# Kernel optimization log

Hardware: AMD Instinct MI355X
Metric: run time of the kernel (lower is better)

Reference implementation:

```python
import jax, jax.numpy as jnp
import numpy as np

N, L, IN = 256, 128, 8
H1, H2, OUT = 768, 512, 1


def setup_inputs() -> dict:
    key = jax.random.key(0)
    ks = jax.random.split(key, 13)
    s = 0.02
    p = lambda k, shape: jax.random.normal(k, shape, dtype=jnp.float32) * s
    return {
        "x": jax.random.normal(ks[0], (N, L, IN), dtype=jnp.float32),
        "W_ih1": p(ks[1], (4 * H1, IN + 1)),
        "b_ih1": p(ks[2], (4 * H1,)),
        "W_hh1": p(ks[3], (4 * H1, H1)),
        "b_hh1": p(ks[4], (4 * H1,)),
        "W_ih2": p(ks[5], (4 * H1, H1)),
        "b_ih2": p(ks[6], (4 * H1,)),
        "W_hh2": p(ks[7], (4 * H1, H1)),
        "b_hh2": p(ks[8], (4 * H1,)),
        "W1": p(ks[9], (H2, H1)),
        "b1": p(ks[10], (H2,)),
        "W2": p(ks[11], (OUT, H2)),
        "b2": p(ks[12], (OUT,)),
    }


def _lstm_cell(inp, h, c, W_ih, b_ih, W_hh, b_hh):
    # PyTorch LSTMCell: gates ordered (input, forget, cell, output)
    g = inp @ W_ih.T + b_ih + h @ W_hh.T + b_hh
    i, f, gg, o = jnp.split(g, 4, axis=-1)
    c = jax.nn.sigmoid(f) * c + jax.nn.sigmoid(i) * jnp.tanh(gg)
    h = jax.nn.sigmoid(o) * jnp.tanh(c)
    return h, c


def reference(x, W_ih1, b_ih1, W_hh1, b_hh1, W_ih2, b_ih2, W_hh2, b_hh2, W1, b1, W2, b2):
    Nb = x.shape[0]
    H = W_hh1.shape[1]
    z = jnp.zeros((Nb, H), x.dtype)
    col0 = jnp.zeros((Nb, 1), x.dtype)  # initial_output = initial_implied_storage = 0

    def step(carry, x_t):  # x_t: (N, IN)
        h1, c1, h2, c2, prev_out, prev_store = carry
        cur_store = prev_store + x_t[:, :1] - prev_out  # (N, 1)
        inp = jnp.concatenate([x_t, cur_store], axis=-1)  # (N, IN+1)
        h1, c1 = _lstm_cell(inp, h1, c1, W_ih1, b_ih1, W_hh1, b_hh1)
        h2, c2 = _lstm_cell(h1, h2, c2, W_ih2, b_ih2, W_hh2, b_hh2)
        # dropout_prob = 0 -> dropout layers are identity
        out = jax.nn.relu(h2 @ W1.T + b1) @ W2.T + b2  # (N, 1)
        return (h1, c1, h2, c2, out, cur_store), (out, cur_store)

    _, (outs, stores) = jax.lax.scan(step, (z, z, z, z, col0, col0), jnp.swapaxes(x, 0, 1))
    # (L, N, 1) -> (N, L, 1)
    return jnp.swapaxes(outs, 0, 1), jnp.swapaxes(stores, 0, 1)
```

## Files before the change

### kernel.cpp

```cpp
#include <hip/hip_runtime.h>

typedef unsigned short u16;
typedef unsigned int u32;
typedef __attribute__((ext_vector_type(8))) unsigned short ushort8;
typedef __attribute__((ext_vector_type(4))) float f32x4;
typedef __attribute__((ext_vector_type(2))) float f32x2;
typedef __attribute__((ext_vector_type(4))) unsigned int u32x4;
typedef __attribute__((ext_vector_type(8))) __bf16 bf16x8;

#define N_B 256
#define LSEQ 128
#define AROW 2304
#define NBLK 256

#define MFMA_B16(a, b, c) __builtin_amdgcn_mfma_f32_16x16x32_bf16( \
    __builtin_bit_cast(bf16x8, a), __builtin_bit_cast(bf16x8, b), c, 0, 0, 0)

#define GLLDS(gp, lp) __builtin_amdgcn_global_load_lds( \
    (const __attribute__((address_space(1))) void*)(gp), \
    (__attribute__((address_space(3))) void*)(lp), 16, 0, 0)
#define GLLDS_C(gp, lp) __builtin_amdgcn_global_load_lds( \
    (const __attribute__((address_space(1))) void*)(gp), \
    (__attribute__((address_space(3))) void*)(lp), 16, 0, 17)

#define ATOMIC_LD(p) __hip_atomic_load((p), __ATOMIC_RELAXED, __HIP_MEMORY_SCOPE_AGENT)
#define ATOMIC_ST(p, v) __hip_atomic_store((p), (v), __ATOMIC_RELAXED, __HIP_MEMORY_SCOPE_AGENT)

__device__ __forceinline__ void st16_sc(void* p, u32x4 v) {
  asm volatile("global_store_dwordx4 %0, %1, off sc0 sc1" :: "v"(p), "v"(v) : "memory");
}

#define OFF_BP2   0ull
#define SZ_BP2    (48ull*192*512*2)
#define OFF_BP1   (OFF_BP2 + SZ_BP2)
#define SZ_BP1    (24ull*192*512*2)
#define OFF_W1P   (OFF_BP1 + SZ_BP1)
#define SZ_W1P    (24ull*32*512*2)
#define OFF_WIH1T (OFF_W1P + SZ_W1P)
#define SZ_WIH1T  (9ull*3072*4)
#define OFF_BS1   (OFF_WIH1T + SZ_WIH1T)
#define OFF_BS2   (OFF_BS1 + 3072*4)
#define OFF_W8Q   (OFF_BS2 + 3072*4)
#define OFF_G1P   (OFF_W8Q + 3072*4)
#define SZ_G1P    (256ull*3072*4)
#define OFF_PBUF  (OFF_G1P + SZ_G1P)
#define SZ_PBUF   (256ull*8*4)
#define OFF_ZERO  (OFF_PBUF + SZ_PBUF)
#define OFF_ACAT  OFF_ZERO
#define SZ_ACAT   (256ull*2304*2)
#define OFF_C1    (OFF_ACAT + SZ_ACAT)
#define OFF_C2    (OFF_C1 + 256ull*768*4)
#define OFF_SB    (OFF_C2 + 256ull*768*4)
#define OFF_BAR   (OFF_SB + 1024)
#define SZ_BAR    (128 + 256*32*4)
#define OFF_END   (OFF_BAR + SZ_BAR)
#define ZERO_BYTES (OFF_END - OFF_ZERO)

__device__ __forceinline__ float sigf(float v) { return 1.f / (1.f + __expf(-v)); }
__device__ __forceinline__ float tanhfast(float v) { return 1.f - 2.f / (__expf(2.f * v) + 1.f); }
__device__ __forceinline__ u16 f2bf(float f) {
  union { float f; unsigned u; } v; v.f = f;
  unsigned r = v.u + 0x7fffu + ((v.u >> 16) & 1u);
  return (u16)(r >> 16);
}

struct Params {
  const float* x;
  const u16* Bp2; const u16* Bp1; const u16* W1p;
  const float* Wih1t; const float* bs1; const float* bs2; const float* w8q;
  const float* b1; const float* W2; const float* b2;
  u16* Acat; float* g1q; float* c1; float* c2; float* sb; float* pbuf;
  unsigned* bar;
  float* outs; float* stores;
};

__device__ __forceinline__ void waitflags(const unsigned* f, int n, unsigned target, int tid) {
  if (tid < 64) {
    for (;;) {
      unsigned v = (tid < n) ? ATOMIC_LD(f + tid) : target;
      if (__all((int)(v >= target))) break;
      __builtin_amdgcn_s_sleep(1);
    }
  }
  __syncthreads();
}
__device__ __forceinline__ void setflag(unsigned* f, unsigned v) {
  asm volatile("s_waitcnt vmcnt(0)" ::: "memory");
  __syncthreads();
  if (threadIdx.x == 0) ATOMIC_ST(f, v);
}

__global__ void pack_kernel(const float* __restrict__ Wih1, const float* __restrict__ bih1,
                            const float* __restrict__ Whh1, const float* __restrict__ bhh1,
                            const float* __restrict__ Wih2, const float* __restrict__ bih2,
                            const float* __restrict__ Whh2, const float* __restrict__ bhh2,
                            const float* __restrict__ W1,
                            u16* __restrict__ Bp2, u16* __restrict__ Bp1, u16* __restrict__ W1p,
                            float* __restrict__ Wih1t, float* __restrict__ bs1,
                            float* __restrict__ bs2, float* __restrict__ w8q) {
  const long NB2 = 48l * 192 * 512, NB1 = 24l * 192 * 512, NW1 = 24l * 32 * 512, NT = 9l * 3072;
  const long total = NB2 + NB1 + NW1 + NT + 3072 * 3;
  for (long idx = (long)blockIdx.x * 256 + threadIdx.x; idx < total; idx += (long)gridDim.x * 256) {
    if (idx < NB2) {
      long kt = idx / (192 * 512); long r = idx % (192 * 512);
      int jt = (int)(r / 512); int s = (int)(r % 512);
      int ll = s >> 3, e = s & 7;
      int k = (int)kt * 32 + ((ll >> 4) * 8) + e;
      int j = jt * 16 + (ll & 15);
      float v = (k < 768) ? Wih2[j * 768 + k] : Whh2[j * 768 + k - 768];
      Bp2[idx] = f2bf(v);
    } else if (idx < NB2 + NB1) {
      long i = idx - NB2;
      long kt = i / (192 * 512); long r = i % (192 * 512);
      int jt = (int)(r / 512); int s = (int)(r % 512);
      int ll = s >> 3, e = s & 7;
      int k = (int)kt * 32 + ((ll >> 4) * 8) + e;
      int j = jt * 16 + (ll & 15);
      Bp1[i] = f2bf(Whh1[j * 768 + k]);
    } else if (idx < NB2 + NB1 + NW1) {
      long i = idx - NB2 - NB1;
      long kt = i / (32 * 512); long r = i % (32 * 512);
      int jt = (int)(r / 512); int s = (int)(r % 512);
      int ll = s >> 3, e = s & 7;
      int k = (int)kt * 32 + ((ll >> 4) * 8) + e;
      int j = jt * 16 + (ll & 15);
      W1p[i] = f2bf(W1[j * 768 + k]);
    } else if (idx < NB2 + NB1 + NW1 + NT) {
      long i = idx - NB2 - NB1 - NW1;
      int k = (int)(i / 3072), j = (int)(i % 3072);
      Wih1t[i] = Wih1[j * 9 + k];
    } else {
      long i = idx - NB2 - NB1 - NW1 - NT;
      if (i < 3072) bs1[i] = bih1[i] + bhh1[i];
      else if (i < 6144) { long j = i - 3072; bs2[j] = bih2[j] + bhh2[j]; }
      else {
        long cq = i - 6144; int cc = (int)(cq >> 2), q = (int)(cq & 3);
        w8q[cq] = Wih1[(q * 768 + cc) * 9 + 8];
      }
    }
  }
}

__global__ __launch_bounds__(256) void lstm_fused(Params P) {
  __shared__ ushort8 sbuf[48 * 64];
  __shared__ float xsb[64][8];
  __shared__ float csh[8];
  float (*fbuf)[64][16] = (float(*)[64][16])sbuf;
  const int tid = threadIdx.x, l = tid & 63, w = tid >> 6;
  const int bid = blockIdx.x;
  const int c = bid >> 6, local = bid & 63;
  const int rowbase = c * 64;
  unsigned* cfl = P.bar + 32 + c * 128;

  if (local < 48) {
    const int mg = local;
    setflag(cfl + local, 1u);
    for (int t = 0; t < 128; ++t) {
      const int rdbase = 768 + (t & 1) * 768;
      const int wrbase = 768 + ((t + 1) & 1) * 768;
      auto stage_g2 = [&](int kc, int slot) {
#pragma unroll
        for (int i = 0; i < 4; ++i) {
          int f = w * 4 + i;
          if (f < 8) {
            int kt2 = f >> 2, rt = f & 3, kt = kc * 2 + kt2;
            int col = (kt >= 24) ? (rdbase + (kt - 24) * 32 + ((l >> 4) * 8))
                                 : (kt * 32 + ((l >> 4) * 8));
            const u16* gp = P.Acat + (rowbase + rt * 16 + (l & 15)) * AROW + col;
            GLLDS_C(gp, &sbuf[(slot * 16 + f) * 64]);
          } else {
            int g = f - 8, kt2 = g >> 2, q = g & 3, kt = kc * 2 + kt2;
            const u16* gp = P.Bp2 + (((long)(kt * 192 + q * 48 + mg)) << 9) + l * 8;
            GLLDS(gp, &sbuf[(slot * 16 + f) * 64]);
          }
        }
      };
      auto kc_of = [](int g) { int k = g + 12; return (k >= 24) ? k - 24 : k; };
      waitflags(cfl, 48, (unsigned)(t + 1), tid);
      f32x4 acc[4] = {};
      stage_g2(kc_of(0), 0);
      stage_g2(kc_of(1), 1);
      for (int g = 0; g < 24; ++g) {
        if (g < 22) {
          if (g == 10) waitflags(cfl + 96, 16, (unsigned)(t + 1), tid);
          stage_g2(kc_of(g + 2), (g + 2) % 3);
          asm volatile("s_waitcnt vmcnt(8)" ::: "memory");
        } else if (g == 22) {
          asm volatile("s_waitcnt vmcnt(4)" ::: "memory");
        } else {
          asm volatile("s_waitcnt vmcnt(0)" ::: "memory");
        }
        __builtin_amdgcn_s_barrier();
        __builtin_amdgcn_sched_barrier(0);
        const int base = (g % 3) * 16;
#pragma unroll
        for (int kt2 = 0; kt2 < 2; ++kt2) {
          ushort8 bfr = sbuf[(base + 8 + kt2 * 4 + w) * 64 + l];
#pragma unroll
          for (int rt = 0; rt < 4; ++rt) {
            ushort8 a = sbuf[(base + kt2 * 4 + rt) * 64 + l];
            acc[rt] = MFMA_B16(a, bfr, acc[rt]);
          }
        }
        __builtin_amdgcn_sched_barrier(0);
        __builtin_amdgcn_s_barrier();
      }
#pragma unroll
      for (int rt = 0; rt < 4; ++rt)
#pragma unroll
        for (int reg = 0; reg < 4; ++reg) {
          int rl = rt * 16 + (l >> 4) * 4 + reg;
          fbuf[w][rl][l & 15] = acc[rt][reg] + P.bs2[w * 768 + mg * 16 + (l & 15)];
        }
      __syncthreads();
      for (int p = tid; p < 128; p += 256) {
        int r = p >> 1, half = p & 1;
        int n = rowbase + r, mG = mg * 16 + half * 8;
        f32x4 cold0 = *(const f32x4*)(P.c2 + n * 768 + mG);
        f32x4 cold1 = *(const f32x4*)(P.c2 + n * 768 + mG + 4);
        u32 hp[4];
        f32x4 cnew0, cnew1;
#pragma unroll
        for (int k = 0; k < 8; ++k) {
          int pp = half * 8 + k;
          float gi = fbuf[0][r][pp], gf = fbuf[1][r][pp], gg = fbuf[2][r][pp], go = fbuf[3][r][pp];
          float co = (k < 4) ? cold0[k] : cold1[k - 4];
          float cn = sigf(gf) * co + sigf(gi) * tanhfast(gg);
          float h = sigf(go) * tanhfast(cn);
          if (k < 4) cnew0[k] = cn; else cnew1[k - 4] = cn;
          if (k & 1) hp[k >> 1] |= ((u32)f2bf(h)) << 16; else hp[k >> 1] = f2bf(h);
        }
        *(f32x4*)(P.c2 + n * 768 + mG) = cnew0;
        *(f32x4*)(P.c2 + n * 768 + mG + 4) = cnew1;
        st16_sc(P.Acat + n * AROW + wrbase + mG, *(u32x4*)hp);
      }
      setflag(cfl + local, (unsigned)(t + 2));

      if (local < 32) {
        waitflags(cfl, 48, (unsigned)(t + 2), tid);
        ushort8* fst = sbuf + 1024;
        const int n0f = rowbase + (local >> 3) * 16, cg2 = local & 7, ctg = cg2 * 4 + w;
        const int h2rd = 768 + ((t + 1) & 1) * 768;
#pragma unroll
        for (int i = 0; i < 6; ++i) {
          int cc = w * 6 + i;
          const u16* gp = P.Acat + (n0f + (l & 15)) * AROW + h2rd + cc * 32 + ((l >> 4) * 8);
          GLLDS_C(gp, &fst[cc * 64]);
        }
        asm volatile("s_waitcnt vmcnt(0)" ::: "memory");
        __syncthreads();
        const u16* bbase = P.W1p + ((long)ctg << 9) + l * 8;
        f32x4 facc = {};
#pragma unroll 6
        for (int kt = 0; kt < 24; ++kt) {
          ushort8 a = fst[kt * 64 + l];
          ushort8 bf8 = *reinterpret_cast<const ushort8*>(bbase + kt * 16384);
          facc = MFMA_B16(a, bf8, facc);
        }
        int col = ctg * 16 + (l & 15);
        float w2v = P.W2[col], b1v = P.b1[col];
        float pr[4];
#pragma unroll
        for (int reg = 0; reg < 4; ++reg) pr[reg] = fmaxf(facc[reg] + b1v, 0.f) * w2v;
#pragma unroll
        for (int mm = 1; mm < 16; mm <<= 1)
#pragma unroll
          for (int reg = 0; reg < 4; ++reg) pr[reg] += __shfl_xor(pr[reg], mm);
        if ((l & 15) == 0)
#pragma unroll
          for (int reg = 0; reg < 4; ++reg) fbuf[w][(l >> 4) * 4 + reg][0] = pr[reg];
        __syncthreads();
        if (tid < 16)
          ATOMIC_ST(P.pbuf + (n0f + tid) * 8 + cg2,
                    fbuf[0][tid][0] + fbuf[1][tid][0] + fbuf[2][tid][0] + fbuf[3][tid][0]);
        setflag(cfl + 64 + local, (unsigned)(t + 2));
      }
    }
  } else {
    const int jb = local - 48;
    const int n0 = rowbase + jb * 4;
    const int quad = jb >> 2;
    for (int t = -1; t < 128; ++t) {
      if (t < 127) {
        if (t >= 0) waitflags(cfl + 96, 16, (unsigned)(t + 1), tid);
        for (int p = tid; p < 512; p += 256)
          xsb[p >> 3][p & 7] = P.x[((rowbase + (p >> 3)) * LSEQ + t + 1) * 8 + (p & 7)];
        __syncthreads();
        f32x4 acc[3][4] = {};
        if (t >= 0) {
          auto stage_g1 = [&](int kt, int slot) {
#pragma unroll
            for (int i = 0; i < 4; ++i) {
              int f = w * 4 + i;
              if (f < 4) {
                const u16* gp = P.Acat + (rowbase + f * 16 + (l & 15)) * AROW + kt * 32 + ((l >> 4) * 8);
                GLLDS_C(gp, &sbuf[(slot * 16 + f) * 64]);
              } else {
                int jt_l = f - 4;
                const u16* gp = P.Bp1 + (((long)(kt * 192 + jb * 12 + jt_l)) << 9) + l * 8;
                GLLDS(gp, &sbuf[(slot * 16 + f) * 64]);
              }
            }
          };
          stage_g1(0, 0);
          stage_g1(1, 1);
          for (int kt = 0; kt < 24; ++kt) {
            if (kt < 22) {
              stage_g1(kt + 2, (kt + 2) % 3);
              asm volatile("s_waitcnt vmcnt(8)" ::: "memory");
            } else if (kt == 22) {
              asm volatile("s_waitcnt vmcnt(4)" ::: "memory");
            } else {
              asm volatile("s_waitcnt vmcnt(0)" ::: "memory");
            }
            __builtin_amdgcn_s_barrier();
            __builtin_amdgcn_sched_barrier(0);
            const int base = (kt % 3) * 16;
            ushort8 a_[4];
#pragma unroll
            for (int rt = 0; rt < 4; ++rt) a_[rt] = sbuf[(base + rt) * 64 + l];
#pragma unroll
            for (int jj = 0; jj < 3; ++jj) {
              ushort8 bfr = sbuf[(base + 4 + w * 3 + jj) * 64 + l];
#pragma unroll
              for (int rt = 0; rt < 4; ++rt)
                acc[jj][rt] = MFMA_B16(a_[rt], bfr, acc[jj][rt]);
            }
            __builtin_amdgcn_sched_barrier(0);
            __builtin_amdgcn_s_barrier();
          }
        }
        float wc[3][8], bsv[3];
#pragma unroll
        for (int jj = 0; jj < 3; ++jj) {
          int ct = jb * 12 + w * 3 + jj;
          int col = ct * 16 + (l & 15);
          bsv[jj] = P.bs1[col];
#pragma unroll
          for (int k = 0; k < 8; ++k) wc[jj][k] = P.Wih1t[k * 3072 + col];
        }
#pragma unroll
        for (int rt = 0; rt < 4; ++rt)
#pragma unroll
          for (int reg = 0; reg < 4; ++reg) {
            int rl = rt * 16 + (l >> 4) * 4 + reg;
            int n = rowbase + rl;
            float xv[8];
#pragma unroll
            for (int k = 0; k < 8; ++k) xv[k] = xsb[rl][k];
#pragma unroll
            for (int jj = 0; jj < 3; ++jj) {
              int ct = jb * 12 + w * 3 + jj;
              int cin = (ct - quad * 48) * 16 + (l & 15);
              float v = acc[jj][rt][reg] + bsv[jj];
#pragma unroll
              for (int k = 0; k < 8; ++k) v += xv[k] * wc[jj][k];
              ATOMIC_ST(P.g1q + n * 3072 + cin * 4 + quad, v);
            }
          }
        setflag(cfl + 48 + jb, (unsigned)(t + 2));
      }

      if (t < 127) {
        waitflags(cfl + 48, 16, (unsigned)(t + 2), tid);
#pragma unroll
        for (int i = 0; i < 12; ++i) {
          int f = w * 12 + i;
          const float* gp = P.g1q + n0 * 3072 + f * 256 + l * 4;
          GLLDS_C(gp, (char*)sbuf + f * 1024);
        }
      }
      float ov = 0.f;
      if (t >= 0) {
        waitflags(cfl + 64, 32, (unsigned)(t + 2), tid);
        if (tid < 4) {
          int n = n0 + tid;
          float pb[8];
#pragma unroll
          for (int i = 0; i < 8; ++i) pb[i] = ATOMIC_LD(P.pbuf + n * 8 + i);
          ov = ((pb[0] + pb[1]) + (pb[2] + pb[3])) + ((pb[4] + pb[5]) + (pb[6] + pb[7])) + P.b2[0];
          P.outs[n * LSEQ + t] = ov;
        }
      }
      if (t < 127) {
        if (tid < 4) {
          int n = n0 + tid;
          float cs = P.sb[n] + P.x[(n * LSEQ + t + 1) * 8] - ov;
          P.sb[n] = cs;
          P.stores[n * LSEQ + t + 1] = cs;
          csh[tid] = cs;
        }
        asm volatile("s_waitcnt vmcnt(0)" ::: "memory");
        __syncthreads();
        const int r = tid >> 6, l2 = tid & 63;
        const int n = n0 + r;
        const float* ldsrow = (const float*)sbuf + r * 3072;
        float cs = csh[r];
#pragma unroll
        for (int ci = 0; ci < 6; ++ci) {
          int m = ci * 128 + l2 * 2;
          f32x4 qa = *(const f32x4*)(ldsrow + m * 4);
          f32x4 qb = *(const f32x4*)(ldsrow + m * 4 + 4);
          f32x4 wa = *(const f32x4*)(P.w8q + m * 4);
          f32x4 wb = *(const f32x4*)(P.w8q + m * 4 + 4);
          float ga[4], gb[4];
#pragma unroll
          for (int q = 0; q < 4; ++q) { ga[q] = qa[q] + cs * wa[q]; gb[q] = qb[q] + cs * wb[q]; }
          f32x2 co = *(const f32x2*)(P.c1 + n * 768 + m);
          float cn0 = sigf(ga[1]) * co.x + sigf(ga[0]) * tanhfast(ga[2]);
          float cn1 = sigf(gb[1]) * co.y + sigf(gb[0]) * tanhfast(gb[2]);
          float h0 = sigf(ga[3]) * tanhfast(cn0);
          float h1 = sigf(gb[3]) * tanhfast(cn1);
          f32x2 cn; cn.x = cn0; cn.y = cn1;
          *(f32x2*)(P.c1 + n * 768 + m) = cn;
          u32 pk = (u32)f2bf(h0) | ((u32)f2bf(h1) << 16);
          ATOMIC_ST((u32*)(P.Acat + n * AROW + m), pk);
        }
        setflag(cfl + 96 + jb, (unsigned)(t + 2));
      }
    }
  }
}

extern "C" void kernel_launch(void* const* d_in, const int* in_sizes, int n_in,
                              void* d_out, int out_size, void* d_ws, size_t ws_size,
                              hipStream_t stream) {
  const float* x    = (const float*)d_in[0];
  const float* Wih1 = (const float*)d_in[1];
  const float* bih1 = (const float*)d_in[2];
  const float* Whh1 = (const float*)d_in[3];
  const float* bhh1 = (const float*)d_in[4];
  const float* Wih2 = (const float*)d_in[5];
  const float* bih2 = (const float*)d_in[6];
  const float* Whh2 = (const float*)d_in[7];
  const float* bhh2 = (const float*)d_in[8];
  const float* W1   = (const float*)d_in[9];
  const float* b1   = (const float*)d_in[10];
  const float* W2   = (const float*)d_in[11];
  const float* b2   = (const float*)d_in[12];

  char* ws = (char*)d_ws;
  u16* Bp2 = (u16*)(ws + OFF_BP2);
  u16* Bp1 = (u16*)(ws + OFF_BP1);
  u16* W1p = (u16*)(ws + OFF_W1P);
  float* Wih1t = (float*)(ws + OFF_WIH1T);
  float* bs1 = (float*)(ws + OFF_BS1);
  float* bs2 = (float*)(ws + OFF_BS2);
  float* w8q = (float*)(ws + OFF_W8Q);
  float* g1q = (float*)(ws + OFF_G1P);
  float* pbuf = (float*)(ws + OFF_PBUF);
  u16* Acat = (u16*)(ws + OFF_ACAT);
  float* c1 = (float*)(ws + OFF_C1);
  float* c2 = (float*)(ws + OFF_C2);
  float* sb = (float*)(ws + OFF_SB);
  unsigned* bar = (unsigned*)(ws + OFF_BAR);
  float* outs = (float*)d_out;
  float* stores = outs + N_B * LSEQ;

  pack_kernel<<<2048, 256, 0, stream>>>(Wih1, bih1, Whh1, bhh1, Wih2, bih2, Whh2, bhh2, W1,
                                        Bp2, Bp1, W1p, Wih1t, bs1, bs2, w8q);
  (void)hipMemsetAsync(ws + OFF_ZERO, 0, ZERO_BYTES, stream);

  Params Pr = {x, Bp2, Bp1, W1p, Wih1t, bs1, bs2, w8q, b1, W2, b2,
               Acat, g1q, c1, c2, sb, pbuf, bar, outs, stores};
  lstm_fused<<<NBLK, 256, 0, stream>>>(Pr);
}
```

Before: 3.820 ms.

## Move output MLP into layer-1 blocks and stage gate writes through LDS

```diff
diff --git a/kernel.cpp b/kernel.cpp
--- a/kernel.cpp
+++ b/kernel.cpp
@@ -43,9 +43,7 @@
 #define OFF_W8Q   (OFF_BS2 + 3072*4)
 #define OFF_G1P   (OFF_W8Q + 3072*4)
 #define SZ_G1P    (256ull*3072*4)
-#define OFF_PBUF  (OFF_G1P + SZ_G1P)
-#define SZ_PBUF   (256ull*8*4)
-#define OFF_ZERO  (OFF_PBUF + SZ_PBUF)
+#define OFF_ZERO  (OFF_G1P + SZ_G1P)
 #define OFF_ACAT  OFF_ZERO
 #define SZ_ACAT   (256ull*2304*2)
 #define OFF_C1    (OFF_ACAT + SZ_ACAT)
@@ -69,7 +67,7 @@
   const u16* Bp2; const u16* Bp1; const u16* W1p;
   const float* Wih1t; const float* bs1; const float* bs2; const float* w8q;
   const float* b1; const float* W2; const float* b2;
-  u16* Acat; float* g1q; float* c1; float* c2; float* sb; float* pbuf;
+  u16* Acat; float* g1q; float* c1; float* c2; float* sb;
   unsigned* bar;
   float* outs; float* stores;
 };
@@ -144,6 +142,8 @@
 __global__ __launch_bounds__(256) void lstm_fused(Params P) {
   __shared__ ushort8 sbuf[48 * 64];
   __shared__ float xsb[64][8];
+  __shared__ u16 h2s[4][768];
+  __shared__ float red[4][4];
   __shared__ float csh[8];
   float (*fbuf)[64][16] = (float(*)[64][16])sbuf;
   const int tid = threadIdx.x, l = tid & 63, w = tid >> 6;
@@ -235,51 +235,10 @@
         st16_sc(P.Acat + n * AROW + wrbase + mG, *(u32x4*)hp);
       }
       setflag(cfl + local, (unsigned)(t + 2));
-
-      if (local < 32) {
-        waitflags(cfl, 48, (unsigned)(t + 2), tid);
-        ushort8* fst = sbuf + 1024;
-        const int n0f = rowbase + (local >> 3) * 16, cg2 = local & 7, ctg = cg2 * 4 + w;
-        const int h2rd = 768 + ((t + 1) & 1) * 768;
-#pragma unroll
-        for (int i = 0; i < 6; ++i) {
-          int cc = w * 6 + i;
-          const u16* gp = P.Acat + (n0f + (l & 15)) * AROW + h2rd + cc * 32 + ((l >> 4) * 8);
-          GLLDS_C(gp, &fst[cc * 64]);
-        }
-        asm volatile("s_waitcnt vmcnt(0)" ::: "memory");
-        __syncthreads();
-        const u16* bbase = P.W1p + ((long)ctg << 9) + l * 8;
-        f32x4 facc = {};
-#pragma unroll 6
-        for (int kt = 0; kt < 24; ++kt) {
-          ushort8 a = fst[kt * 64 + l];
-          ushort8 bf8 = *reinterpret_cast<const ushort8*>(bbase + kt * 16384);
-          facc = MFMA_B16(a, bf8, facc);
-        }
-        int col = ctg * 16 + (l & 15);
-        float w2v = P.W2[col], b1v = P.b1[col];
-        float pr[4];
-#pragma unroll
-        for (int reg = 0; reg < 4; ++reg) pr[reg] = fmaxf(facc[reg] + b1v, 0.f) * w2v;
-#pragma unroll
-        for (int mm = 1; mm < 16; mm <<= 1)
-#pragma unroll
-          for (int reg = 0; reg < 4; ++reg) pr[reg] += __shfl_xor(pr[reg], mm);
-        if ((l & 15) == 0)
-#pragma unroll
-          for (int reg = 0; reg < 4; ++reg) fbuf[w][(l >> 4) * 4 + reg][0] = pr[reg];
-        __syncthreads();
-        if (tid < 16)
-          ATOMIC_ST(P.pbuf + (n0f + tid) * 8 + cg2,
-                    fbuf[0][tid][0] + fbuf[1][tid][0] + fbuf[2][tid][0] + fbuf[3][tid][0]);
-        setflag(cfl + 64 + local, (unsigned)(t + 2));
-      }
     }
   } else {
     const int jb = local - 48;
     const int n0 = rowbase + jb * 4;
-    const int quad = jb >> 2;
     for (int t = -1; t < 128; ++t) {
       if (t < 127) {
         if (t >= 0) waitflags(cfl + 96, 16, (unsigned)(t + 1), tid);
@@ -297,7 +256,8 @@
                 GLLDS_C(gp, &sbuf[(slot * 16 + f) * 64]);
               } else {
                 int jt_l = f - 4;
-                const u16* gp = P.Bp1 + (((long)(kt * 192 + jb * 12 + jt_l)) << 9) + l * 8;
+                int q = jt_l / 3, jj = jt_l - q * 3;
+                const u16* gp = P.Bp1 + (((long)(kt * 192 + q * 48 + jb * 3 + jj)) << 9) + l * 8;
                 GLLDS(gp, &sbuf[(slot * 16 + f) * 64]);
               }
             }
@@ -333,35 +293,38 @@
         float wc[3][8], bsv[3];
 #pragma unroll
         for (int jj = 0; jj < 3; ++jj) {
-          int ct = jb * 12 + w * 3 + jj;
-          int col = ct * 16 + (l & 15);
-          bsv[jj] = P.bs1[col];
-#pragma unroll
-          for (int k = 0; k < 8; ++k) wc[jj][k] = P.Wih1t[k * 3072 + col];
-        }
+          int j = w * 768 + (jb * 3 + jj) * 16 + (l & 15);
+          bsv[jj] = P.bs1[j];
+#pragma unroll
+          for (int k = 0; k < 8; ++k) wc[jj][k] = P.Wih1t[k * 3072 + j];
+        }
+        float* eps = (float*)sbuf;
 #pragma unroll
         for (int rt = 0; rt < 4; ++rt)
 #pragma unroll
           for (int reg = 0; reg < 4; ++reg) {
             int rl = rt * 16 + (l >> 4) * 4 + reg;
-            int n = rowbase + rl;
             float xv[8];
 #pragma unroll
             for (int k = 0; k < 8; ++k) xv[k] = xsb[rl][k];
 #pragma unroll
             for (int jj = 0; jj < 3; ++jj) {
-              int ct = jb * 12 + w * 3 + jj;
-              int cin = (ct - quad * 48) * 16 + (l & 15);
               float v = acc[jj][rt][reg] + bsv[jj];
 #pragma unroll
               for (int k = 0; k < 8; ++k) v += xv[k] * wc[jj][k];
-              ATOMIC_ST(P.g1q + n * 3072 + cin * 4 + quad, v);
+              eps[rl * 192 + (jj * 16 + (l & 15)) * 4 + w] = v;
             }
           }
+        __syncthreads();
+#pragma unroll
+        for (int k2 = 0; k2 < 12; ++k2) {
+          int idx = tid + k2 * 256;
+          int row = idx / 48, cl = idx - row * 48;
+          u32x4 v = *(const u32x4*)(eps + row * 192 + cl * 4);
+          st16_sc(P.g1q + (rowbase + row) * 3072 + (jb * 48 + cl) * 4, v);
+        }
         setflag(cfl + 48 + jb, (unsigned)(t + 2));
-      }
-
-      if (t < 127) {
+
         waitflags(cfl + 48, 16, (unsigned)(t + 2), tid);
 #pragma unroll
         for (int i = 0; i < 12; ++i) {
@@ -370,51 +333,90 @@
           GLLDS_C(gp, (char*)sbuf + f * 1024);
         }
       }
-      float ov = 0.f;
+
       if (t >= 0) {
-        waitflags(cfl + 64, 32, (unsigned)(t + 2), tid);
-        if (tid < 4) {
-          int n = n0 + tid;
-          float pb[8];
-#pragma unroll
-          for (int i = 0; i < 8; ++i) pb[i] = ATOMIC_LD(P.pbuf + n * 8 + i);
-          ov = ((pb[0] + pb[1]) + (pb[2] + pb[3])) + ((pb[4] + pb[5]) + (pb[6] + pb[7])) + P.b2[0];
+        waitflags(cfl, 48, (unsigned)(t + 2), tid);
+        const int h2rd = 768 + ((t + 1) & 1) * 768;
+        for (int i = w; i < 6; i += 4) {
+          int bo = i * 1024 + l * 16;
+          int row = bo / 1536, cb = bo - row * 1536;
+          const u16* gp = P.Acat + (n0 + row) * AROW + h2rd + cb / 2;
+          GLLDS_C(gp, (char*)h2s + i * 1024);
+        }
+        asm volatile("s_waitcnt vmcnt(0)" ::: "memory");
+        __syncthreads();
+        f32x4 fa[8] = {};
+        const u16* bb = P.W1p + l * 8;
+        for (int kt = 0; kt < 24; ++kt) {
+          ushort8 a = *(const ushort8*)((const char*)h2s + (l & 3) * 1536 + kt * 64 + ((l >> 4) * 8) * 2);
+#pragma unroll
+          for (int i = 0; i < 8; ++i) {
+            ushort8 b = *(const ushort8*)(bb + (((long)kt * 32 + (w * 8 + i)) << 9));
+            fa[i] = MFMA_B16(a, b, fa[i]);
+          }
+        }
+        float pr[4] = {0.f, 0.f, 0.f, 0.f};
+#pragma unroll
+        for (int i = 0; i < 8; ++i) {
+          int col = (w * 8 + i) * 16 + (l & 15);
+          float b1v = P.b1[col], w2v = P.W2[col];
+#pragma unroll
+          for (int reg = 0; reg < 4; ++reg)
+            pr[reg] += fmaxf(fa[i][reg] + b1v, 0.f) * w2v;
+        }
+#pragma unroll
+        for (int mm = 1; mm < 16; mm <<= 1)
+#pragma unroll
+          for (int reg = 0; reg < 4; ++reg) pr[reg] += __shfl_xor(pr[reg], mm);
+        if (l == 0)
+#pragma unroll
+          for (int reg = 0; reg < 4; ++reg) red[w][reg] = pr[reg];
+        __syncthreads();
+      }
+
+      if (tid < 4) {
+        int n = n0 + tid;
+        float ov = 0.f;
+        if (t >= 0) {
+          ov = red[0][tid] + red[1][tid] + red[2][tid] + red[3][tid] + P.b2[0];
           P.outs[n * LSEQ + t] = ov;
         }
-      }
-      if (t < 127) {
-        if (tid < 4) {
-          int n = n0 + tid;
+        if (t < 127) {
           float cs = P.sb[n] + P.x[(n * LSEQ + t + 1) * 8] - ov;
           P.sb[n] = cs;
           P.stores[n * LSEQ + t + 1] = cs;
           csh[tid] = cs;
         }
+      }
+      if (t < 127) {
         asm volatile("s_waitcnt vmcnt(0)" ::: "memory");
         __syncthreads();
         const int r = tid >> 6, l2 = tid & 63;
         const int n = n0 + r;
         const float* ldsrow = (const float*)sbuf + r * 3072;
         float cs = csh[r];
-#pragma unroll
-        for (int ci = 0; ci < 6; ++ci) {
-          int m = ci * 128 + l2 * 2;
-          f32x4 qa = *(const f32x4*)(ldsrow + m * 4);
-          f32x4 qb = *(const f32x4*)(ldsrow + m * 4 + 4);
-          f32x4 wa = *(const f32x4*)(P.w8q + m * 4);
-          f32x4 wb = *(const f32x4*)(P.w8q + m * 4 + 4);
-          float ga[4], gb[4];
-#pragma unroll
-          for (int q = 0; q < 4; ++q) { ga[q] = qa[q] + cs * wa[q]; gb[q] = qb[q] + cs * wb[q]; }
-          f32x2 co = *(const f32x2*)(P.c1 + n * 768 + m);
-          float cn0 = sigf(ga[1]) * co.x + sigf(ga[0]) * tanhfast(ga[2]);
-          float cn1 = sigf(gb[1]) * co.y + sigf(gb[0]) * tanhfast(gb[2]);
-          float h0 = sigf(ga[3]) * tanhfast(cn0);
-          float h1 = sigf(gb[3]) * tanhfast(cn1);
-          f32x2 cn; cn.x = cn0; cn.y = cn1;
-          *(f32x2*)(P.c1 + n * 768 + m) = cn;
-          u32 pk = (u32)f2bf(h0) | ((u32)f2bf(h1) << 16);
-          ATOMIC_ST((u32*)(P.Acat + n * AROW + m), pk);
+        for (int idx = l2; idx < 96; idx += 64) {
+          int m = idx * 8;
+          u32 hp[4];
+          f32x4 c1v0 = *(const f32x4*)(P.c1 + n * 768 + m);
+          f32x4 c1v1 = *(const f32x4*)(P.c1 + n * 768 + m + 4);
+          f32x4 nc0, nc1;
+#pragma unroll
+          for (int k = 0; k < 8; ++k) {
+            int mm = m + k;
+            f32x4 q = *(const f32x4*)(ldsrow + mm * 4);
+            f32x4 wq = *(const f32x4*)(P.w8q + mm * 4);
+            float g0 = q[0] + cs * wq[0], g1v = q[1] + cs * wq[1];
+            float g2v = q[2] + cs * wq[2], g3v = q[3] + cs * wq[3];
+            float co = (k < 4) ? c1v0[k] : c1v1[k - 4];
+            float cn = sigf(g1v) * co + sigf(g0) * tanhfast(g2v);
+            float h = sigf(g3v) * tanhfast(cn);
+            if (k < 4) nc0[k] = cn; else nc1[k - 4] = cn;
+            if (k & 1) hp[k >> 1] |= ((u32)f2bf(h)) << 16; else hp[k >> 1] = f2bf(h);
+          }
+          *(f32x4*)(P.c1 + n * 768 + m) = nc0;
+          *(f32x4*)(P.c1 + n * 768 + m + 4) = nc1;
+          st16_sc(P.Acat + n * AROW + m, *(u32x4*)hp);
         }
         setflag(cfl + 96 + jb, (unsigned)(t + 2));
       }
@@ -448,7 +450,6 @@
   float* bs2 = (float*)(ws + OFF_BS2);
   float* w8q = (float*)(ws + OFF_W8Q);
   float* g1q = (float*)(ws + OFF_G1P);
-  float* pbuf = (float*)(ws + OFF_PBUF);
   u16* Acat = (u16*)(ws + OFF_ACAT);
   float* c1 = (float*)(ws + OFF_C1);
   float* c2 = (float*)(ws + OFF_C2);
@@ -462,6 +463,6 @@
   (void)hipMemsetAsync(ws + OFF_ZERO, 0, ZERO_BYTES, stream);
 
   Params Pr = {x, Bp2, Bp1, W1p, Wih1t, bs1, bs2, w8q, b1, W2, b2,
-               Acat, g1q, c1, c2, sb, pbuf, bar, outs, stores};
+               Acat, g1q, c1, c2, sb, bar, outs, stores};
   lstm_fused<<<NBLK, 256, 0, stream>>>(Pr);
 }
```

New measurement: 13.36 ms. 250% more time.

## Load B operands into registers with deeper pipelines and vectorize gate1 stores

Applied to the files above, without the earlier changes.

```diff
diff --git a/kernel.cpp b/kernel.cpp
--- a/kernel.cpp
+++ b/kernel.cpp
@@ -29,6 +29,8 @@
 __device__ __forceinline__ void st16_sc(void* p, u32x4 v) {
   asm volatile("global_store_dwordx4 %0, %1, off sc0 sc1" :: "v"(p), "v"(v) : "memory");
 }
+#define LOADB(dst, gp) asm volatile("global_load_dwordx4 %0, %1, off" : "=v"(dst) : "v"(gp))
+#define VMW(N) asm volatile("s_waitcnt vmcnt(" #N ")" ::: "memory")
 
 #define OFF_BP2   0ull
 #define SZ_BP2    (48ull*192*512*2)
@@ -158,53 +160,65 @@
     for (int t = 0; t < 128; ++t) {
       const int rdbase = 768 + (t & 1) * 768;
       const int wrbase = 768 + ((t + 1) & 1) * 768;
-      auto stage_g2 = [&](int kc, int slot) {
-#pragma unroll
-        for (int i = 0; i < 4; ++i) {
-          int f = w * 4 + i;
-          if (f < 8) {
-            int kt2 = f >> 2, rt = f & 3, kt = kc * 2 + kt2;
-            int col = (kt >= 24) ? (rdbase + (kt - 24) * 32 + ((l >> 4) * 8))
-                                 : (kt * 32 + ((l >> 4) * 8));
-            const u16* gp = P.Acat + (rowbase + rt * 16 + (l & 15)) * AROW + col;
-            GLLDS_C(gp, &sbuf[(slot * 16 + f) * 64]);
-          } else {
-            int g = f - 8, kt2 = g >> 2, q = g & 3, kt = kc * 2 + kt2;
-            const u16* gp = P.Bp2 + (((long)(kt * 192 + q * 48 + mg)) << 9) + l * 8;
-            GLLDS(gp, &sbuf[(slot * 16 + f) * 64]);
-          }
+      waitflags(cfl, 48, (unsigned)(t + 1), tid);
+
+      f32x4 acc[4] = {};
+      ushort8 bring[4][2];
+      auto issueA2 = [&](int gi) {
+        const int slot = gi % 6;
+#pragma unroll
+        for (int kt2 = 0; kt2 < 2; ++kt2) {
+          int kt = ((gi < 12) ? gi + 12 : gi - 12) * 2 + kt2;
+          int col = (kt >= 24) ? (rdbase + (kt - 24) * 32 + ((l >> 4) * 8))
+                               : (kt * 32 + ((l >> 4) * 8));
+          const u16* gp = P.Acat + (rowbase + w * 16 + (l & 15)) * AROW + col;
+          GLLDS_C(gp, &sbuf[slot * 512 + (kt2 * 4 + w) * 64]);
         }
       };
-      auto kc_of = [](int g) { int k = g + 12; return (k >= 24) ? k - 24 : k; };
-      waitflags(cfl, 48, (unsigned)(t + 1), tid);
-      f32x4 acc[4] = {};
-      stage_g2(kc_of(0), 0);
-      stage_g2(kc_of(1), 1);
-      for (int g = 0; g < 24; ++g) {
-        if (g < 22) {
-          if (g == 10) waitflags(cfl + 96, 16, (unsigned)(t + 1), tid);
-          stage_g2(kc_of(g + 2), (g + 2) % 3);
-          asm volatile("s_waitcnt vmcnt(8)" ::: "memory");
-        } else if (g == 22) {
-          asm volatile("s_waitcnt vmcnt(4)" ::: "memory");
-        } else {
-          asm volatile("s_waitcnt vmcnt(0)" ::: "memory");
-        }
+      auto baddr2 = [&](int gi, int kt2) -> const u16* {
+        int kt = ((gi < 12) ? gi + 12 : gi - 12) * 2 + kt2;
+        return P.Bp2 + (((long)(kt * 192 + w * 48 + mg)) << 9) + l * 8;
+      };
+      auto g2_step = [&](int g, const ushort8 (&bu)[2]) {
         __builtin_amdgcn_s_barrier();
         __builtin_amdgcn_sched_barrier(0);
-        const int base = (g % 3) * 16;
-#pragma unroll
-        for (int kt2 = 0; kt2 < 2; ++kt2) {
-          ushort8 bfr = sbuf[(base + 8 + kt2 * 4 + w) * 64 + l];
+        const int sb8 = (g % 6) * 512;
+#pragma unroll
+        for (int kt2 = 0; kt2 < 2; ++kt2)
 #pragma unroll
           for (int rt = 0; rt < 4; ++rt) {
-            ushort8 a = sbuf[(base + kt2 * 4 + rt) * 64 + l];
-            acc[rt] = MFMA_B16(a, bfr, acc[rt]);
+            ushort8 a = sbuf[sb8 + (kt2 * 4 + rt) * 64 + l];
+            acc[rt] = MFMA_B16(a, bu[kt2], acc[rt]);
           }
-        }
         __builtin_amdgcn_sched_barrier(0);
-        __builtin_amdgcn_s_barrier();
-      }
+      };
+#pragma unroll
+      for (int p = 0; p < 3; ++p) {
+        issueA2(p);
+        LOADB(bring[p][0], baddr2(p, 0));
+        LOADB(bring[p][1], baddr2(p, 1));
+      }
+      for (int ko = 0; ko < 5; ++ko) {
+#pragma unroll
+        for (int u = 0; u < 4; ++u) {
+          const int g = ko * 4 + u;
+          if (g == 9) waitflags(cfl + 96, 16, (unsigned)(t + 1), tid);
+          issueA2(g + 3);
+          LOADB(bring[(u + 3) & 3][0], baddr2(g + 3, 0));
+          LOADB(bring[(u + 3) & 3][1], baddr2(g + 3, 1));
+          VMW(12);
+          g2_step(g, bring[u]);
+        }
+      }
+      issueA2(23);
+      LOADB(bring[3][0], baddr2(23, 0));
+      LOADB(bring[3][1], baddr2(23, 1));
+      VMW(12); g2_step(20, bring[0]);
+      VMW(8);  g2_step(21, bring[1]);
+      VMW(4);  g2_step(22, bring[2]);
+      VMW(0);  g2_step(23, bring[3]);
+      __syncthreads();
+
 #pragma unroll
       for (int rt = 0; rt < 4; ++rt)
 #pragma unroll
@@ -279,8 +293,8 @@
   } else {
     const int jb = local - 48;
     const int n0 = rowbase + jb * 4;
-    const int quad = jb >> 2;
     for (int t = -1; t < 128; ++t) {
+      float ov = 0.f;
       if (t < 127) {
         if (t >= 0) waitflags(cfl + 96, 16, (unsigned)(t + 1), tid);
         for (int p = tid; p < 512; p += 256)
@@ -288,80 +302,92 @@
         __syncthreads();
         f32x4 acc[3][4] = {};
         if (t >= 0) {
-          auto stage_g1 = [&](int kt, int slot) {
-#pragma unroll
-            for (int i = 0; i < 4; ++i) {
-              int f = w * 4 + i;
-              if (f < 4) {
-                const u16* gp = P.Acat + (rowbase + f * 16 + (l & 15)) * AROW + kt * 32 + ((l >> 4) * 8);
-                GLLDS_C(gp, &sbuf[(slot * 16 + f) * 64]);
-              } else {
-                int jt_l = f - 4;
-                const u16* gp = P.Bp1 + (((long)(kt * 192 + jb * 12 + jt_l)) << 9) + l * 8;
-                GLLDS(gp, &sbuf[(slot * 16 + f) * 64]);
-              }
-            }
+          ushort8 br1[4][3];
+          auto issueA1 = [&](int ki) {
+            const u16* gp = P.Acat + (rowbase + w * 16 + (l & 15)) * AROW + ki * 32 + ((l >> 4) * 8);
+            GLLDS_C(gp, &sbuf[(ki & 7) * 256 + w * 64]);
           };
-          stage_g1(0, 0);
-          stage_g1(1, 1);
-          for (int kt = 0; kt < 24; ++kt) {
-            if (kt < 22) {
-              stage_g1(kt + 2, (kt + 2) % 3);
-              asm volatile("s_waitcnt vmcnt(8)" ::: "memory");
-            } else if (kt == 22) {
-              asm volatile("s_waitcnt vmcnt(4)" ::: "memory");
-            } else {
-              asm volatile("s_waitcnt vmcnt(0)" ::: "memory");
-            }
+          auto baddr1 = [&](int ki, int jj) -> const u16* {
+            return P.Bp1 + (((long)(ki * 192 + w * 48 + jb * 3 + jj)) << 9) + l * 8;
+          };
+          auto g1_step = [&](int kt, const ushort8 (&bu)[3]) {
             __builtin_amdgcn_s_barrier();
             __builtin_amdgcn_sched_barrier(0);
-            const int base = (kt % 3) * 16;
+            const int sb8 = (kt & 7) * 256;
             ushort8 a_[4];
 #pragma unroll
-            for (int rt = 0; rt < 4; ++rt) a_[rt] = sbuf[(base + rt) * 64 + l];
-#pragma unroll
-            for (int jj = 0; jj < 3; ++jj) {
-              ushort8 bfr = sbuf[(base + 4 + w * 3 + jj) * 64 + l];
+            for (int rt = 0; rt < 4; ++rt) a_[rt] = sbuf[sb8 + rt * 64 + l];
+#pragma unroll
+            for (int jj = 0; jj < 3; ++jj)
 #pragma unroll
               for (int rt = 0; rt < 4; ++rt)
-                acc[jj][rt] = MFMA_B16(a_[rt], bfr, acc[jj][rt]);
+                acc[jj][rt] = MFMA_B16(a_[rt], bu[jj], acc[jj][rt]);
+            __builtin_amdgcn_sched_barrier(0);
+          };
+#pragma unroll
+          for (int p = 0; p < 3; ++p) {
+            issueA1(p);
+            LOADB(br1[p][0], baddr1(p, 0));
+            LOADB(br1[p][1], baddr1(p, 1));
+            LOADB(br1[p][2], baddr1(p, 2));
+          }
+          for (int ko = 0; ko < 5; ++ko) {
+#pragma unroll
+            for (int u = 0; u < 4; ++u) {
+              const int kt = ko * 4 + u;
+              issueA1(kt + 3);
+              LOADB(br1[(u + 3) & 3][0], baddr1(kt + 3, 0));
+              LOADB(br1[(u + 3) & 3][1], baddr1(kt + 3, 1));
+              LOADB(br1[(u + 3) & 3][2], baddr1(kt + 3, 2));
+              VMW(12);
+              g1_step(kt, br1[u]);
             }
-            __builtin_amdgcn_sched_barrier(0);
-            __builtin_amdgcn_s_barrier();
           }
+          issueA1(23);
+          LOADB(br1[3][0], baddr1(23, 0));
+          LOADB(br1[3][1], baddr1(23, 1));
+          LOADB(br1[3][2], baddr1(23, 2));
+          VMW(12); g1_step(20, br1[0]);
+          VMW(8);  g1_step(21, br1[1]);
+          VMW(4);  g1_step(22, br1[2]);
+          VMW(0);  g1_step(23, br1[3]);
+          __syncthreads();
         }
         float wc[3][8], bsv[3];
 #pragma unroll
         for (int jj = 0; jj < 3; ++jj) {
-          int ct = jb * 12 + w * 3 + jj;
-          int col = ct * 16 + (l & 15);
-          bsv[jj] = P.bs1[col];
-#pragma unroll
-          for (int k = 0; k < 8; ++k) wc[jj][k] = P.Wih1t[k * 3072 + col];
-        }
+          int j = w * 768 + (jb * 3 + jj) * 16 + (l & 15);
+          bsv[jj] = P.bs1[j];
+#pragma unroll
+          for (int k = 0; k < 8; ++k) wc[jj][k] = P.Wih1t[k * 3072 + j];
+        }
+        float* eps = (float*)sbuf;
 #pragma unroll
         for (int rt = 0; rt < 4; ++rt)
 #pragma unroll
           for (int reg = 0; reg < 4; ++reg) {
             int rl = rt * 16 + (l >> 4) * 4 + reg;
-            int n = rowbase + rl;
             float xv[8];
 #pragma unroll
             for (int k = 0; k < 8; ++k) xv[k] = xsb[rl][k];
 #pragma unroll
             for (int jj = 0; jj < 3; ++jj) {
-              int ct = jb * 12 + w * 3 + jj;
-              int cin = (ct - quad * 48) * 16 + (l & 15);
               float v = acc[jj][rt][reg] + bsv[jj];
 #pragma unroll
               for (int k = 0; k < 8; ++k) v += xv[k] * wc[jj][k];
-              ATOMIC_ST(P.g1q + n * 3072 + cin * 4 + quad, v);
+              eps[rl * 192 + (jj * 16 + (l & 15)) * 4 + w] = v;
             }
           }
+        __syncthreads();
+#pragma unroll
+        for (int k2 = 0; k2 < 12; ++k2) {
+          int idx = tid + k2 * 256;
+          int row = idx / 48, cl = idx - row * 48;
+          u32x4 v = *(const u32x4*)(eps + row * 192 + cl * 4);
+          st16_sc(P.g1q + (rowbase + row) * 3072 + (jb * 48 + cl) * 4, v);
+        }
         setflag(cfl + 48 + jb, (unsigned)(t + 2));
-      }
-
-      if (t < 127) {
+
         waitflags(cfl + 48, 16, (unsigned)(t + 2), tid);
 #pragma unroll
         for (int i = 0; i < 12; ++i) {
@@ -370,7 +396,7 @@
           GLLDS_C(gp, (char*)sbuf + f * 1024);
         }
       }
-      float ov = 0.f;
+
       if (t >= 0) {
         waitflags(cfl + 64, 32, (unsigned)(t + 2), tid);
         if (tid < 4) {
@@ -396,25 +422,28 @@
         const int n = n0 + r;
         const float* ldsrow = (const float*)sbuf + r * 3072;
         float cs = csh[r];
-#pragma unroll
-        for (int ci = 0; ci < 6; ++ci) {
-          int m = ci * 128 + l2 * 2;
-          f32x4 qa = *(const f32x4*)(ldsrow + m * 4);
-          f32x4 qb = *(const f32x4*)(ldsrow + m * 4 + 4);
-          f32x4 wa = *(const f32x4*)(P.w8q + m * 4);
-          f32x4 wb = *(const f32x4*)(P.w8q + m * 4 + 4);
-          float ga[4], gb[4];
-#pragma unroll
-          for (int q = 0; q < 4; ++q) { ga[q] = qa[q] + cs * wa[q]; gb[q] = qb[q] + cs * wb[q]; }
-          f32x2 co = *(const f32x2*)(P.c1 + n * 768 + m);
-          float cn0 = sigf(ga[1]) * co.x + sigf(ga[0]) * tanhfast(ga[2]);
-          float cn1 = sigf(gb[1]) * co.y + sigf(gb[0]) * tanhfast(gb[2]);
-          float h0 = sigf(ga[3]) * tanhfast(cn0);
-          float h1 = sigf(gb[3]) * tanhfast(cn1);
-          f32x2 cn; cn.x = cn0; cn.y = cn1;
-          *(f32x2*)(P.c1 + n * 768 + m) = cn;
-          u32 pk = (u32)f2bf(h0) | ((u32)f2bf(h1) << 16);
-          ATOMIC_ST((u32*)(P.Acat + n * AROW + m), pk);
+        for (int idx = l2; idx < 96; idx += 64) {
+          int m = idx * 8;
+          u32 hp[4];
+          f32x4 c1v0 = *(const f32x4*)(P.c1 + n * 768 + m);
+          f32x4 c1v1 = *(const f32x4*)(P.c1 + n * 768 + m + 4);
+          f32x4 nc0, nc1;
+#pragma unroll
+          for (int k = 0; k < 8; ++k) {
+            int mm = m + k;
+            f32x4 q = *(const f32x4*)(ldsrow + mm * 4);
+            f32x4 wq = *(const f32x4*)(P.w8q + mm * 4);
+            float g0 = q[0] + cs * wq[0], g1v = q[1] + cs * wq[1];
+            float g2v = q[2] + cs * wq[2], g3v = q[3] + cs * wq[3];
+            float co = (k < 4) ? c1v0[k] : c1v1[k - 4];
+            float cn = sigf(g1v) * co + sigf(g0) * tanhfast(g2v);
+            float h = sigf(g3v) * tanhfast(cn);
+            if (k < 4) nc0[k] = cn; else nc1[k - 4] = cn;
+            if (k & 1) hp[k >> 1] |= ((u32)f2bf(h)) << 16; else hp[k >> 1] = f2bf(h);
+          }
+          *(f32x4*)(P.c1 + n * 768 + m) = nc0;
+          *(f32x4*)(P.c1 + n * 768 + m + 4) = nc1;
+          st16_sc(P.Acat + n * AROW + m, *(u32x4*)hp);
         }
         setflag(cfl + 96 + jb, (unsigned)(t + 2));
       }
```

Result: faster. 3.159 ms (-17.3%).
